# Kernel tuning notes

Hardware: AMD Instinct MI355X
Metric: run time of the kernel (lower is better)

Reference implementation:

```python
import jax, jax.numpy as jnp
import numpy as np

B, S, D_MODEL, D_FF = 4, 2048, 1024, 4096


def setup_inputs() -> dict:
    key = jax.random.key(0)
    ks = jax.random.split(key, 8)
    return {
        "x": jax.random.normal(ks[0], (B, S, D_MODEL), dtype=jnp.float32),
        "W1": jax.random.normal(ks[1], (D_MODEL, D_FF), dtype=jnp.float32) * (1.0 / np.sqrt(D_MODEL)),
        "b1": jnp.zeros((D_FF,), dtype=jnp.float32),
        "quantum_phases": jax.random.normal(ks[2], (D_FF,), dtype=jnp.float32) * (2.0 * np.pi),
        "quantum_weights_real": jax.random.normal(ks[3], (D_FF,), dtype=jnp.float32) * 0.1,
        "quantum_weights_imag": jax.random.normal(ks[4], (D_FF,), dtype=jnp.float32) * 0.1,
        "W2": jax.random.normal(ks[5], (D_FF, D_MODEL), dtype=jnp.float32) * (1.0 / np.sqrt(D_FF)),
        "b2": jnp.zeros((D_MODEL,), dtype=jnp.float32),
    }


def _quantum_transform(hidden, theta, w_real, w_imag):
    # hidden: [B,S,d_ff]; theta/w_real/w_imag: [d_ff] broadcast over channels
    imag = w_imag * jnp.sin(theta + hidden * 0.1)
    quantum_phase = jnp.cos(theta) * w_real + jnp.sin(theta) * w_imag  # [d_ff]
    return hidden + quantum_phase * imag * 0.1


def reference(x, W1, b1, quantum_phases, quantum_weights_real, quantum_weights_imag, W2, b2):
    hidden = jnp.einsum("bsd,df->bsf", x, W1) + b1  # [B,S,d_ff]
    q = _quantum_transform(hidden, quantum_phases, quantum_weights_real, quantum_weights_imag)
    act = jax.nn.relu(q)  # dropout is identity in eval mode
    return jnp.einsum("bsf,fd->bsd", act, W2) + b2
```

## Files before the change

kernel.cpp:

```cpp
#include <hip/hip_runtime.h>

typedef __bf16 bf16x8 __attribute__((ext_vector_type(8)));
typedef short  s16x8  __attribute__((ext_vector_type(8)));
typedef float  f32x4  __attribute__((ext_vector_type(4)));

#define DEVINL __device__ __forceinline__

DEVINL unsigned short f2bf(float f) {
  unsigned int u = __builtin_bit_cast(unsigned int, f);
  u += 0x7fffu + ((u >> 16) & 1u);
  return (unsigned short)(u >> 16);
}

DEVINL void async16(const void* g, void* l) {
  __builtin_amdgcn_global_load_lds(
      (const __attribute__((address_space(1))) unsigned int*)g,
      (__attribute__((address_space(3))) unsigned int*)l, 16, 0, 0);
}


__global__ void cvt_f32_bf16(const float* __restrict__ in,
                             unsigned short* __restrict__ out, int n4) {
  int i = blockIdx.x * blockDim.x + threadIdx.x;
  int stride = gridDim.x * blockDim.x;
  for (; i < n4; i += stride) {
    float4 v = ((const float4*)in)[i];
    ushort4 o;
    o.x = f2bf(v.x); o.y = f2bf(v.y); o.z = f2bf(v.z); o.w = f2bf(v.w);
    ((ushort4*)out)[i] = o;
  }
}

__global__ void transpose_cvt(const float* __restrict__ in,
                              unsigned short* __restrict__ out, int R, int C) {
  __shared__ unsigned short tile[32][33];
  int bc = blockIdx.x * 32, br = blockIdx.y * 32;
  int tx = threadIdx.x & 31, ty = threadIdx.x >> 5;
#pragma unroll
  for (int i = 0; i < 32; i += 8)
    tile[ty + i][tx] = f2bf(in[(size_t)(br + ty + i) * C + (bc + tx)]);
  __syncthreads();
#pragma unroll
  for (int i = 0; i < 32; i += 8)
    out[(size_t)(bc + ty + i) * R + (br + tx)] = tile[tx][ty + i];
}

__global__ void qconst(const float* __restrict__ theta,
                       const float* __restrict__ wre,
                       const float* __restrict__ wim,
                       float* __restrict__ c1, int n) {
  int i = blockIdx.x * blockDim.x + threadIdx.x;
  if (i < n) {
    float t = theta[i];
    c1[i] = (cosf(t) * wre[i] + sinf(t) * wim[i]) * wim[i] * 0.1f;
  }
}


template <int BM, int BN, int NT, bool FUSED>
__global__ __launch_bounds__(512, 2) void gemm8p(
    const unsigned short* __restrict__ A,
    const unsigned short* __restrict__ Bt,
    const float* __restrict__ bias,
    const float* __restrict__ theta,
    const float* __restrict__ c1,
    void* __restrict__ Cout,
    int N, int nTilesN) {
  constexpr int K      = NT * 64;
  constexpr int WROWS  = BM / 2;
  constexpr int M_REP  = WROWS / 16;
  constexpr int MH     = M_REP / 2;
  constexpr int ABYTES = BM * 128;
  constexpr int BUF    = (BM + BN) * 128;
  constexpr int LA     = ABYTES / 8192;
  constexpr int LB     = BN * 128 / 8192;
  static_assert(LB == 4 && (LA == 4 || LA == 2), "geometry");

  __shared__ __align__(16) char lds[2 * BUF];

  int nwg = gridDim.x;
  int wg = blockIdx.x;
  int sw = (wg & 7) * (nwg >> 3) + (wg >> 3);
  int rowBase = (sw / nTilesN) * BM;
  int colBase = (sw % nTilesN) * BN;

  const int t = threadIdx.x;
  const int lane = t & 63;
  const int wid = t >> 6;
  const int wr = wid >> 2, wc = wid & 3;
  const int lr = lane & 15;
  const int lg = lane >> 4;
  const int r7 = lane & 7;

  const int arow = t >> 3;
  const int acolB = ((t & 7) * 16) ^ ((arow & 7) << 4);
  const unsigned short* aSrc = A  + (size_t)(rowBase + arow) * K + (acolB >> 1);
  const unsigned short* bSrc = Bt + (size_t)(colBase + arow) * K + (acolB >> 1);

  const int aRd = (wr * WROWS + lr) * 128 + ((lg ^ r7) * 16);
  const int bRd = ABYTES + (wc * 64 + lr) * 128 + ((lg ^ r7) * 16);

  f32x4 acc[M_REP][4] = {};
  bf16x8 a[MH][2], b[4][2];

#define STAGE_A(T1, BO, j)                                                  \
  async16(aSrc + ((size_t)(j) * 64 * K + (size_t)(T1) * 64),                \
          &lds[(BO) + (j) * 8192 + t * 16])
#define STAGE_B(T2, BO, j)                                                  \
  async16(bSrc + ((size_t)(j) * 64 * K + (size_t)(T2) * 64),                \
          &lds[(BO) + ABYTES + (j) * 8192 + t * 16])

#define LDS_A(mh, BO)                                                       \
  _Pragma("unroll") for (int mi = 0; mi < MH; ++mi)                         \
  _Pragma("unroll") for (int ks = 0; ks < 2; ++ks)                          \
    a[mi][ks] = __builtin_bit_cast(bf16x8, *(const s16x8*)&lds[             \
        (BO) + ((aRd + ((mh) * MH + mi) * 2048) ^ (ks * 64))])
#define LDS_B(nh, BO)                                                       \
  _Pragma("unroll") for (int nn = 0; nn < 2; ++nn)                          \
  _Pragma("unroll") for (int ks = 0; ks < 2; ++ks)                          \
    b[(nh) * 2 + nn][ks] = __builtin_bit_cast(bf16x8, *(const s16x8*)&lds[  \
        (BO) + ((bRd + ((nh) * 2 + nn) * 2048) ^ (ks * 64))])

#define QUAD(mh, nh)                                                        \
  __builtin_amdgcn_s_setprio(1);                                            \
  _Pragma("unroll") for (int mi = 0; mi < MH; ++mi)                         \
  _Pragma("unroll") for (int nn = 0; nn < 2; ++nn)                          \
  _Pragma("unroll") for (int ks = 0; ks < 2; ++ks)                          \
    acc[(mh) * MH + mi][(nh) * 2 + nn] =                                    \
        __builtin_amdgcn_mfma_f32_16x16x32_bf16(                            \
            a[mi][ks], b[(nh) * 2 + nn][ks],                                \
            acc[(mh) * MH + mi][(nh) * 2 + nn], 0, 0, 0);                   \
  __builtin_amdgcn_s_setprio(0)

#define BAR() __builtin_amdgcn_s_barrier()
#define DRAIN_LGKM() asm volatile("s_waitcnt lgkmcnt(0)" ::: "memory")

#define GROUP(T, BO, OBO) do {                                              \
                                                                \
    LDS_A(0, BO); LDS_B(0, BO);                                             \
    if ((T) + 1 < NT) {                                                     \
      _Pragma("unroll") for (int j = 0; j < LA; ++j)                        \
        STAGE_A((T) + 1, OBO, j);                                           \
    }                                                                       \
    QUAD(0, 0);                                                             \
    LDS_B(1, BO);                                                           \
    QUAD(0, 1);                                                             \
    DRAIN_LGKM();                                                           \
    BAR();                                                                  \
                                                                \
    LDS_A(1, BO);                                                           \
    if ((T) + 2 < NT) {                                                     \
      _Pragma("unroll") for (int j = 0; j < LB; ++j)                        \
        STAGE_B((T) + 2, BO, j);                                            \
    }                                                                       \
    QUAD(1, 0);                                                             \
    QUAD(1, 1);                                                             \
    DRAIN_LGKM();                                                           \
    if ((T) < NT - 2) {                                                     \
      asm volatile("s_waitcnt vmcnt(4)" ::: "memory");                      \
    } else if ((T) == NT - 2) {                                             \
      asm volatile("s_waitcnt vmcnt(0)" ::: "memory");                      \
    }                                                                       \
    BAR();                                                                  \
  } while (0)

#pragma unroll
  for (int j = 0; j < LA; ++j) STAGE_A(0, 0, j);
#pragma unroll
  for (int j = 0; j < LB; ++j) STAGE_B(0, 0, j);
#pragma unroll
  for (int j = 0; j < LB; ++j) STAGE_B(1, BUF, j);
  asm volatile("s_waitcnt vmcnt(4)" ::: "memory");
  BAR();

  for (int T = 0; T < NT; T += 2) {
    GROUP(T, 0, BUF);
    GROUP(T + 1, BUF, 0);
  }

#undef GROUP
#undef QUAD
#undef LDS_A
#undef LDS_B
#undef STAGE_A
#undef STAGE_B
#undef BAR
#undef DRAIN_LGKM

  const int orow0 = rowBase + wr * WROWS + (lane >> 4) * 4;
  const int ocol0 = colBase + wc * 64 + lr;
#pragma unroll
  for (int ni = 0; ni < 4; ++ni) {
    int n = ocol0 + ni * 16;
    float bv = bias[n];
    float th = 0.f, cc = 0.f;
    if constexpr (FUSED) { th = theta[n]; cc = c1[n]; }
#pragma unroll
    for (int mi = 0; mi < M_REP; ++mi) {
#pragma unroll
      for (int r = 0; r < 4; ++r) {
        size_t m = (size_t)(orow0 + mi * 16 + r);
        float h = acc[mi][ni][r] + bv;
        if constexpr (FUSED) {
          float q = h + cc * __sinf(th + 0.1f * h);
          ((unsigned short*)Cout)[m * N + n] = f2bf(fmaxf(q, 0.f));
        } else {
          ((float*)Cout)[m * N + n] = h;
        }
      }
    }
  }
}


extern "C" void kernel_launch(void* const* d_in, const int* in_sizes, int n_in,
                              void* d_out, int out_size, void* d_ws,
                              size_t ws_size, hipStream_t stream) {
  const float* x     = (const float*)d_in[0];
  const float* W1    = (const float*)d_in[1];
  const float* b1    = (const float*)d_in[2];
  const float* theta = (const float*)d_in[3];
  const float* qwr   = (const float*)d_in[4];
  const float* qwi   = (const float*)d_in[5];
  const float* W2    = (const float*)d_in[6];
  const float* b2    = (const float*)d_in[7];
  float* out = (float*)d_out;

  const int M = 4 * 2048;
  const int DM = 1024, DF = 4096;

  size_t need = ((size_t)96 << 20) + DF * sizeof(float);
  if (ws_size < need) return;

  char* ws = (char*)d_ws;
  unsigned short* xb   = (unsigned short*)ws;
  unsigned short* w1t  = (unsigned short*)(ws + ((size_t)16 << 20));
  unsigned short* w2t  = (unsigned short*)(ws + ((size_t)24 << 20));
  unsigned short* actb = (unsigned short*)(ws + ((size_t)32 << 20));
  float* c1 = (float*)(ws + ((size_t)96 << 20));

  cvt_f32_bf16<<<2048, 256, 0, stream>>>(x, xb, M * DM / 4);
  transpose_cvt<<<dim3(DF / 32, DM / 32), 256, 0, stream>>>(W1, w1t, DM, DF);
  transpose_cvt<<<dim3(DM / 32, DF / 32), 256, 0, stream>>>(W2, w2t, DF, DM);
  qconst<<<DF / 256, 256, 0, stream>>>(theta, qwr, qwi, c1, DF);

  gemm8p<256, 256, 16, true><<<512, 512, 0, stream>>>(
      xb, w1t, b1, theta, c1, (void*)actb, DF, DF / 256);
  gemm8p<128, 256, 64, false><<<256, 512, 0, stream>>>(
      actb, w2t, b2, nullptr, nullptr, (void*)out, DM, DM / 256);
}
```

Before: 159.8 us.

## Restructure GEMM main loop into two-window pipeline with prefetched A fragments

Reorganizes the K-loop of both GEMMs so each tile is processed in two windows. The first A half-fragment for the next tile is preloaded from LDS while the current second half computes, and A and B for tile T+2 are staged together into the freed buffer. Each tile's loads are now fully drained with vmcnt(0) before the barrier, replacing the staggered partial waits. The goal is to hide LDS read latency behind MFMA work, at the cost of extra fragment registers and a stricter global-load wait that may expose memory latency.

```diff
diff --git a/kernel.cpp b/kernel.cpp
--- a/kernel.cpp
+++ b/kernel.cpp
@@ -58,7 +58,7 @@
 
 
 template <int BM, int BN, int NT, bool FUSED>
-__global__ __launch_bounds__(512, 2) void gemm8p(
+__global__ __launch_bounds__(512, 2) void gemmsk(
     const unsigned short* __restrict__ A,
     const unsigned short* __restrict__ Bt,
     const float* __restrict__ bias,
@@ -101,7 +101,7 @@
   const int bRd = ABYTES + (wc * 64 + lr) * 128 + ((lg ^ r7) * 16);
 
   f32x4 acc[M_REP][4] = {};
-  bf16x8 a[MH][2], b[4][2];
+  bf16x8 a0[MH][2], a1[MH][2], b[4][2];
 
 #define STAGE_A(T1, BO, j)                                                  \
   async16(aSrc + ((size_t)(j) * 64 * K + (size_t)(T1) * 64),                \
@@ -110,57 +110,59 @@
   async16(bSrc + ((size_t)(j) * 64 * K + (size_t)(T2) * 64),                \
           &lds[(BO) + ABYTES + (j) * 8192 + t * 16])
 
-#define LDS_A(mh, BO)                                                       \
-  _Pragma("unroll") for (int mi = 0; mi < MH; ++mi)                         \
-  _Pragma("unroll") for (int ks = 0; ks < 2; ++ks)                          \
-    a[mi][ks] = __builtin_bit_cast(bf16x8, *(const s16x8*)&lds[             \
-        (BO) + ((aRd + ((mh) * MH + mi) * 2048) ^ (ks * 64))])
-#define LDS_B(nh, BO)                                                       \
+#define LDS_B2(nh, BO)                                                      \
   _Pragma("unroll") for (int nn = 0; nn < 2; ++nn)                          \
   _Pragma("unroll") for (int ks = 0; ks < 2; ++ks)                          \
     b[(nh) * 2 + nn][ks] = __builtin_bit_cast(bf16x8, *(const s16x8*)&lds[  \
         (BO) + ((bRd + ((nh) * 2 + nn) * 2048) ^ (ks * 64))])
-
-#define QUAD(mh, nh)                                                        \
+#define LDS_A0(BO)                                                          \
+  _Pragma("unroll") for (int mi = 0; mi < MH; ++mi)                         \
+  _Pragma("unroll") for (int ks = 0; ks < 2; ++ks)                          \
+    a0[mi][ks] = __builtin_bit_cast(bf16x8, *(const s16x8*)&lds[            \
+        (BO) + ((aRd + mi * 2048) ^ (ks * 64))])
+#define LDS_A1(BO)                                                          \
+  _Pragma("unroll") for (int mi = 0; mi < MH; ++mi)                         \
+  _Pragma("unroll") for (int ks = 0; ks < 2; ++ks)                          \
+    a1[mi][ks] = __builtin_bit_cast(bf16x8, *(const s16x8*)&lds[            \
+        (BO) + ((aRd + (MH + mi) * 2048) ^ (ks * 64))])
+
+#define QUAD(AF, MOFF, nh)                                                  \
   __builtin_amdgcn_s_setprio(1);                                            \
   _Pragma("unroll") for (int mi = 0; mi < MH; ++mi)                         \
   _Pragma("unroll") for (int nn = 0; nn < 2; ++nn)                          \
   _Pragma("unroll") for (int ks = 0; ks < 2; ++ks)                          \
-    acc[(mh) * MH + mi][(nh) * 2 + nn] =                                    \
+    acc[(MOFF) + mi][(nh) * 2 + nn] =                                       \
         __builtin_amdgcn_mfma_f32_16x16x32_bf16(                            \
-            a[mi][ks], b[(nh) * 2 + nn][ks],                                \
-            acc[(mh) * MH + mi][(nh) * 2 + nn], 0, 0, 0);                   \
+            AF[mi][ks], b[(nh) * 2 + nn][ks],                               \
+            acc[(MOFF) + mi][(nh) * 2 + nn], 0, 0, 0);                      \
   __builtin_amdgcn_s_setprio(0)
 
 #define BAR() __builtin_amdgcn_s_barrier()
 #define DRAIN_LGKM() asm volatile("s_waitcnt lgkmcnt(0)" ::: "memory")
-
-#define GROUP(T, BO, OBO) do {                                              \
-                                                                \
-    LDS_A(0, BO); LDS_B(0, BO);                                             \
-    if ((T) + 1 < NT) {                                                     \
+#define DRAIN_VM() asm volatile("s_waitcnt vmcnt(0)" ::: "memory")
+
+#define WIN_A(T, BO) do {                                                   \
+    LDS_B2(0, BO);                                                          \
+    LDS_B2(1, BO);                                                          \
+    LDS_A1(BO);                                                             \
+    QUAD(a0, 0, 0);                                                         \
+    QUAD(a0, 0, 1);                                                         \
+    DRAIN_LGKM();                                                           \
+    DRAIN_VM();                                                             \
+    BAR();                                                                  \
+  } while (0)
+
+#define WIN_B(T, BO, OBO) do {                                              \
+    if ((T) + 2 < NT) {                                                     \
       _Pragma("unroll") for (int j = 0; j < LA; ++j)                        \
-        STAGE_A((T) + 1, OBO, j);                                           \
-    }                                                                       \
-    QUAD(0, 0);                                                             \
-    LDS_B(1, BO);                                                           \
-    QUAD(0, 1);                                                             \
-    DRAIN_LGKM();                                                           \
-    BAR();                                                                  \
-                                                                \
-    LDS_A(1, BO);                                                           \
-    if ((T) + 2 < NT) {                                                     \
+        STAGE_A((T) + 2, BO, j);                                            \
       _Pragma("unroll") for (int j = 0; j < LB; ++j)                        \
         STAGE_B((T) + 2, BO, j);                                            \
     }                                                                       \
-    QUAD(1, 0);                                                             \
-    QUAD(1, 1);                                                             \
+    if ((T) + 1 < NT) LDS_A0(OBO);                                          \
+    QUAD(a1, MH, 0);                                                        \
+    QUAD(a1, MH, 1);                                                        \
     DRAIN_LGKM();                                                           \
-    if ((T) < NT - 2) {                                                     \
-      asm volatile("s_waitcnt vmcnt(4)" ::: "memory");                      \
-    } else if ((T) == NT - 2) {                                             \
-      asm volatile("s_waitcnt vmcnt(0)" ::: "memory");                      \
-    }                                                                       \
     BAR();                                                                  \
   } while (0)
 
@@ -169,23 +171,31 @@
 #pragma unroll
   for (int j = 0; j < LB; ++j) STAGE_B(0, 0, j);
 #pragma unroll
+  for (int j = 0; j < LA; ++j) STAGE_A(1, BUF, j);
+#pragma unroll
   for (int j = 0; j < LB; ++j) STAGE_B(1, BUF, j);
-  asm volatile("s_waitcnt vmcnt(4)" ::: "memory");
+  asm volatile("s_waitcnt vmcnt(%0)" :: "n"(LA + LB) : "memory");
   BAR();
+  LDS_A0(0);
 
   for (int T = 0; T < NT; T += 2) {
-    GROUP(T, 0, BUF);
-    GROUP(T + 1, BUF, 0);
-  }
-
-#undef GROUP
+    WIN_A(T, 0);
+    WIN_B(T, 0, BUF);
+    WIN_A(T + 1, BUF);
+    WIN_B(T + 1, BUF, 0);
+  }
+
+#undef WIN_A
+#undef WIN_B
 #undef QUAD
-#undef LDS_A
-#undef LDS_B
+#undef LDS_A0
+#undef LDS_A1
+#undef LDS_B2
 #undef STAGE_A
 #undef STAGE_B
 #undef BAR
 #undef DRAIN_LGKM
+#undef DRAIN_VM
 
   const int orow0 = rowBase + wr * WROWS + (lane >> 4) * 4;
   const int ocol0 = colBase + wc * 64 + lr;
@@ -244,8 +254,8 @@
   transpose_cvt<<<dim3(DM / 32, DF / 32), 256, 0, stream>>>(W2, w2t, DF, DM);
   qconst<<<DF / 256, 256, 0, stream>>>(theta, qwr, qwi, c1, DF);
 
-  gemm8p<256, 256, 16, true><<<512, 512, 0, stream>>>(
+  gemmsk<256, 256, 16, true><<<512, 512, 0, stream>>>(
       xb, w1t, b1, theta, c1, (void*)actb, DF, DF / 256);
-  gemm8p<128, 256, 64, false><<<256, 512, 0, stream>>>(
+  gemmsk<128, 256, 64, false><<<256, 512, 0, stream>>>(
       actb, w2t, b2, nullptr, nullptr, (void*)out, DM, DM / 256);
 }
```

Result: slower. 282.6 us (median of 2 runs) (+76.9%).
